# Kernel tuning notes

Hardware: AMD Instinct MI355X
Metric: run time of the kernel (lower is better)

The kernel has to match this reference:

```python
import jax, jax.numpy as jnp
import numpy as np

N_NODES = 100000
N_EDGES = 1600000
IN_DIM = 128
HID_DIM = 128
N_MASK = 5000
N_CLASSES = 4


def gcn_layer(x, src, dst, edge_weight, W, b):
    """PyG GCNConv: x' = D^{-1/2} (A + I) D^{-1/2} (x W) + b, with edge weights."""
    n = x.shape[0]
    loop = jnp.arange(n, dtype=src.dtype)
    s = jnp.concatenate([src, loop])                      # [E+N]
    d = jnp.concatenate([dst, loop])                      # [E+N]
    w = jnp.concatenate([edge_weight, jnp.ones((n,), edge_weight.dtype)])
    deg = jax.ops.segment_sum(w, d, num_segments=n)       # weighted in-degree incl. self-loop
    dis = jnp.where(deg > 0, jax.lax.rsqrt(deg), 0.0)     # deg^{-1/2}, inf -> 0
    norm = dis[s] * w * dis[d]                            # [E+N]
    h = x @ W                                             # [N, H] small GEMM
    msg = h[s] * norm[:, None]                            # gather + scale  [E+N, H]
    out = jax.ops.segment_sum(msg, d, num_segments=n)     # scatter-add     [N, H]
    return out + b


def setup_inputs() -> dict:
    key = jax.random.key(0)
    ks = jax.random.split(key, 8)
    x = jax.random.normal(ks[0], (N_NODES, IN_DIM), dtype=jnp.float32)
    edge_weight = jax.random.uniform(ks[1], (N_EDGES,), dtype=jnp.float32)
    W1 = jax.random.normal(ks[2], (IN_DIM, HID_DIM), dtype=jnp.float32) * (1.0 / np.sqrt(IN_DIM))
    b1 = jnp.zeros((HID_DIM,), jnp.float32)
    W2 = jax.random.normal(ks[3], (HID_DIM, HID_DIM), dtype=jnp.float32) * (1.0 / np.sqrt(HID_DIM))
    b2 = jnp.zeros((HID_DIM,), jnp.float32)
    edge_index = jax.random.randint(ks[4], (2, N_EDGES), 0, N_NODES, dtype=jnp.int32)
    mask_idx = jax.random.randint(ks[5], (N_MASK,), 0, N_NODES, dtype=jnp.int32)
    y = jax.random.randint(ks[6], (N_NODES,), 0, N_CLASSES, dtype=jnp.int32)
    return {"x": x, "edge_weight": edge_weight, "W1": W1, "b1": b1,
            "W2": W2, "b2": b2, "edge_index": edge_index,
            "mask_idx": mask_idx, "y": y}


def reference(x, edge_weight, W1, b1, W2, b2, edge_index, mask_idx, y):
    src, dst = edge_index[0], edge_index[1]
    h = gcn_layer(x, src, dst, edge_weight, W1, b1)
    h = jax.nn.relu(h)
    # F.dropout(training=False) in eval mode is identity
    h = gcn_layer(h, src, dst, edge_weight, W2, b2)
    return h[mask_idx], y[mask_idx]
```

## Files before the change

### kernel.cpp

```cpp
#include <hip/hip_runtime.h>

constexpr int N = 100000;
constexpr int E = 1600000;
constexpr int D = 128;
constexpr int M = 5000;

constexpr int MF_BLKS = (N + 255) / 256;

constexpr int NB  = 196;
constexpr int EB  = 2048;
constexpr int NPB = (E + EB - 1) / EB;
constexpr int HL  = NB * NPB;
constexpr int SC_BLKS = (HL + 1023) / 1024;
constexpr int PREP_BLKS = 64;
constexpr int MB_BLKS = (M + 255) / 256;

typedef __attribute__((ext_vector_type(8))) short bf16x8;
typedef __attribute__((ext_vector_type(4))) float f32x4;


__device__ __forceinline__ unsigned int pack_bf16x2(float a, float b) {
    unsigned int ua = __float_as_uint(a);
    unsigned int ub = __float_as_uint(b);
    ua = (ua + 0x7FFFu + ((ua >> 16) & 1u)) >> 16;
    ub = (ub + 0x7FFFu + ((ub >> 16) & 1u)) & 0xFFFF0000u;
    return ua | ub;
}
__device__ __forceinline__ unsigned short bf16_rne(float a) {
    unsigned int ua = __float_as_uint(a);
    return (unsigned short)((ua + 0x7FFFu + ((ua >> 16) & 1u)) >> 16);
}
__device__ __forceinline__ float bf16_lo(unsigned int u) { return __uint_as_float(u << 16); }
__device__ __forceinline__ float bf16_hi(unsigned int u) { return __uint_as_float(u & 0xFFFF0000u); }


__global__ __launch_bounds__(256) void k_misc1(const int* __restrict__ dst,
                                               int* __restrict__ hist,
                                               const float* __restrict__ W1,
                                               unsigned int* __restrict__ Wt1,
                                               const float* __restrict__ W2,
                                               unsigned int* __restrict__ Wt2,
                                               const int* __restrict__ mask,
                                               unsigned int* __restrict__ maskbit,
                                               unsigned int* __restrict__ needed) {
    __shared__ int h[NB];
    const int t = threadIdx.x;
    if (blockIdx.x < NPB) {
        if (t < NB) h[t] = 0;
        __syncthreads();
        const int base = blockIdx.x * EB;
#pragma unroll
        for (int i = 0; i < 8; ++i) {
            int e = base + t + i * 256;
            if (e < E) {
                int b = __builtin_nontemporal_load(dst + e) >> 9;
                atomicAdd(&h[b], 1);
            }
        }
        __syncthreads();
        if (t < NB) hist[t * NPB + blockIdx.x] = h[t];
    } else if (blockIdx.x < NPB + PREP_BLKS) {
        int gi = (blockIdx.x - NPB) * 256 + t;
        const float* W = (gi < 8192) ? W1 : W2;
        unsigned int* Wt = (gi < 8192) ? Wt1 : Wt2;
        int idx = gi & 8191;
        int n = idx >> 6, kk = idx & 63;
        float a = W[(2 * kk) * D + n];
        float b = W[(2 * kk + 1) * D + n];
        Wt[idx] = pack_bf16x2(a, b);
    } else {
        int i = (blockIdx.x - NPB - PREP_BLKS) * 256 + t;
        if (i < M) {
            int n = mask[i];
            atomicOr(&maskbit[n >> 5], 1u << (n & 31));
            atomicOr(&needed[n >> 5], 1u << (n & 31));
        }
    }
}


__global__ __launch_bounds__(256) void k_misc2(const int* __restrict__ hist,
                                               int* __restrict__ bs,
                                               const unsigned int* __restrict__ maskbit,
                                               const int* __restrict__ src,
                                               const int* __restrict__ dst,
                                               unsigned int* __restrict__ needed) {
    __shared__ int ws_[4];
    const int t = threadIdx.x;
    if (blockIdx.x < SC_BLKS) {
        const int idx = blockIdx.x * 1024 + t * 4;
        int s = 0;
        if (idx + 3 < HL) {
            int4 c = *(const int4*)(hist + idx);
            s = c.x + c.y + c.z + c.w;
        } else {
            for (int i = 0; i < 4; ++i) if (idx + i < HL) s += hist[idx + i];
        }
        for (int off = 32; off > 0; off >>= 1) s += __shfl_down(s, off);
        if ((t & 63) == 0) ws_[t >> 6] = s;
        __syncthreads();
        if (t == 0) bs[blockIdx.x] = ws_[0] + ws_[1] + ws_[2] + ws_[3];
    } else {
        const int base = (blockIdx.x - SC_BLKS) * EB;
#pragma unroll
        for (int i = 0; i < 8; ++i) {
            int e = base + t + i * 256;
            if (e < E) {
                int d = __builtin_nontemporal_load(dst + e);
                if ((maskbit[d >> 5] >> (d & 31)) & 1u) {
                    int s = src[e];
                    atomicOr(&needed[s >> 5], 1u << (s & 31));
                }
            }
        }
    }
}


__global__ __launch_bounds__(256) void k_scanf(const int* __restrict__ hist,
                                               const int* __restrict__ bs,
                                               int* __restrict__ histS) {
    __shared__ int sh[256];
    __shared__ int waveS[4];
    const int t = threadIdx.x;
    const int lane = t & 63;
    const int wave = t >> 6;

    sh[t] = (t < SC_BLKS) ? bs[t] : 0;
    __syncthreads();
    for (int off = 1; off < 256; off <<= 1) {
        int u = (t >= off) ? sh[t - off] : 0;
        __syncthreads();
        sh[t] += u;
        __syncthreads();
    }
    const int bOff = sh[blockIdx.x] - bs[blockIdx.x];

    const int idx = blockIdx.x * 1024 + t * 4;
    int4 c = make_int4(0, 0, 0, 0);
    if (idx + 3 < HL) c = *(const int4*)(hist + idx);
    else {
        if (idx + 0 < HL) c.x = hist[idx + 0];
        if (idx + 1 < HL) c.y = hist[idx + 1];
        if (idx + 2 < HL) c.z = hist[idx + 2];
        if (idx + 3 < HL) c.w = hist[idx + 3];
    }
    int s = c.x + c.y + c.z + c.w;

    int v = s;
    for (int off = 1; off < 64; off <<= 1) {
        int u = __shfl_up(v, off);
        if (lane >= off) v += u;
    }
    if (lane == 63) waveS[wave] = v;
    __syncthreads();
    int waveBase = 0;
    for (int w = 0; w < 4; ++w) if (w < wave) waveBase += waveS[w];
    int excl = bOff + waveBase + (v - s);

    int4 rs;
    rs.x = excl;
    rs.y = excl + c.x;
    rs.z = excl + c.x + c.y;
    rs.w = excl + c.x + c.y + c.z;
    if (idx + 3 < HL) {
        *(int4*)(histS + idx) = rs;
    } else {
        if (idx + 0 < HL) histS[idx + 0] = rs.x;
        if (idx + 1 < HL) histS[idx + 1] = rs.y;
        if (idx + 2 < HL) histS[idx + 2] = rs.z;
        if (idx + 3 < HL) histS[idx + 3] = rs.w;
    }
}


union SMem {
    unsigned int Ws[128 * 68];
    struct { int cnt[512]; float wsum[512]; int off[512]; int waveS[4]; } l;
};


template <bool BF16IN>
__device__ __forceinline__ void gemm_mfma_body(unsigned int* __restrict__ Ws,
                                               const void* __restrict__ Xin,
                                               const unsigned int* __restrict__ Wt,
                                               unsigned short* __restrict__ out, int blk) {
    const int t = threadIdx.x;
#pragma unroll
    for (int i = 0; i < 8; ++i) {
        int f4 = t + i * 256;
        int n = f4 >> 4;
        int k4 = f4 & 15;
        uint4 w = ((const uint4*)Wt)[f4];
        *(uint4*)(&Ws[n * 68 + k4 * 4]) = w;
    }
    __syncthreads();

    const int wv = t >> 6, lane = t & 63;
    const int q = lane >> 4, l15 = lane & 15;
    const int rowBase = blk * 256 + wv * 64;

    f32x4 acc[4][8] = {};
#pragma unroll
    for (int kc = 0; kc < 4; ++kc) {
        bf16x8 af[4];
#pragma unroll
        for (int rt = 0; rt < 4; ++rt) {
            int row = rowBase + rt * 16 + l15;
            if (row > N - 1) row = N - 1;
            union { uint4 u; bf16x8 v; } cv;
            if (BF16IN) {
                cv.u = *(const uint4*)((const unsigned int*)Xin + (size_t)row * 64 + kc * 16 + q * 4);
            } else {
                const float* xr = (const float*)Xin + (size_t)row * D + kc * 32 + q * 8;
                float4 x0 = *(const float4*)xr;
                float4 x1 = *(const float4*)(xr + 4);
                cv.u.x = pack_bf16x2(x0.x, x0.y);
                cv.u.y = pack_bf16x2(x0.z, x0.w);
                cv.u.z = pack_bf16x2(x1.x, x1.y);
                cv.u.w = pack_bf16x2(x1.z, x1.w);
            }
            af[rt] = cv.v;
        }
#pragma unroll
        for (int ct = 0; ct < 8; ++ct) {
            union { uint4 u; bf16x8 v; } bv;
            bv.u = *(const uint4*)(&Ws[(ct * 16 + l15) * 68 + kc * 16 + q * 4]);
#pragma unroll
            for (int rt = 0; rt < 4; ++rt)
                acc[rt][ct] = __builtin_amdgcn_mfma_f32_16x16x32_bf16(af[rt], bv.v, acc[rt][ct], 0, 0, 0);
        }
    }

#pragma unroll
    for (int rt = 0; rt < 4; ++rt) {
#pragma unroll
        for (int ct = 0; ct < 8; ++ct) {
            int col = ct * 16 + l15;
#pragma unroll
            for (int r = 0; r < 4; ++r) {
                int row = rowBase + rt * 16 + q * 4 + r;
                if (row < N) out[(size_t)row * D + col] = bf16_rne(acc[rt][ct][r]);
            }
        }
    }
}


__global__ __launch_bounds__(256) void k_part(const int* __restrict__ src,
                                              const int* __restrict__ dst,
                                              const float* __restrict__ ew,
                                              const int* __restrict__ histS,
                                              unsigned long long* __restrict__ tmp) {
    __shared__ int base_[NB];
    const int t = threadIdx.x;
    if (t < NB) base_[t] = histS[t * NPB + blockIdx.x];
    __syncthreads();
    const int eb = blockIdx.x * EB;
#pragma unroll
    for (int i = 0; i < 8; ++i) {
        int e = eb + t + i * 256;
        if (e < E) {
            int d = __builtin_nontemporal_load(dst + e);
            int s = __builtin_nontemporal_load(src + e);
            float w = __builtin_nontemporal_load(ew + e);
            int b = d >> 9;
            int pos = atomicAdd(&base_[b], 1);
            unsigned long long rec =
                ((unsigned long long)(unsigned int)__float_as_int(w) << 32) |
                ((unsigned int)s << 9) | (unsigned int)(d & 511);
            __builtin_nontemporal_store(rec, tmp + pos);
        }
    }
}


__device__ __forceinline__ void local_body(SMem& sm,
                                           const unsigned long long* __restrict__ tmp,
                                           const int* __restrict__ histS,
                                           float* __restrict__ dis,
                                           int* __restrict__ rowStart,
                                           int2* __restrict__ pairs) {
    const int b = blockIdx.x;
    const int t = threadIdx.x;
    const int segBeg = histS[b * NPB];
    const int segEnd = (b + 1 < NB) ? histS[(b + 1) * NPB] : E;

    int*   cnt   = sm.l.cnt;
    float* wsum  = sm.l.wsum;
    int*   off   = sm.l.off;
    int*   waveS = sm.l.waveS;
    cnt[t] = 0; cnt[t + 256] = 0;
    wsum[t] = 0.f; wsum[t + 256] = 0.f;
    __syncthreads();

    for (int e = segBeg + t; e < segEnd; e += 256) {
        unsigned long long rec = tmp[e];
        int dl = (int)(rec & 511);
        float w = __uint_as_float((unsigned int)(rec >> 32));
        atomicAdd(&cnt[dl], 1);
        atomicAdd(&wsum[dl], w);
    }
    __syncthreads();

    const int i0 = t * 2, i1 = t * 2 + 1;
    const int c0 = cnt[i0], c1 = cnt[i1];
    const int pv = c0 + c1;
    const int lane = t & 63, wv = t >> 6;
    int v = pv;
    for (int o = 1; o < 64; o <<= 1) {
        int u = __shfl_up(v, o);
        if (lane >= o) v += u;
    }
    if (lane == 63) waveS[wv] = v;
    __syncthreads();
    int wb = 0;
    for (int w = 0; w < 4; ++w) if (w < wv) wb += waveS[w];
    const int ex = wb + v - pv;
    off[i0] = ex;
    off[i1] = ex + c0;
    const int node0 = b * 512 + i0, node1 = b * 512 + i1;
    if (node0 < N) { rowStart[node0] = segBeg + ex;      dis[node0] = rsqrtf(1.0f + wsum[i0]); }
    if (node1 < N) { rowStart[node1] = segBeg + ex + c0; dis[node1] = rsqrtf(1.0f + wsum[i1]); }
    cnt[i0] = 0; cnt[i1] = 0;
    if (b == NB - 1 && t == 0) rowStart[N] = E;
    __syncthreads();

    for (int e = segBeg + t; e < segEnd; e += 256) {
        unsigned long long rec = tmp[e];
        int dl = (int)(rec & 511);
        int s  = (int)((rec >> 9) & 0xFFFFF);
        unsigned int wbits = (unsigned int)(rec >> 32);
        int r = atomicAdd(&cnt[dl], 1);
        pairs[segBeg + off[dl] + r] = make_int2(s, (int)wbits);
    }
}


__global__ __launch_bounds__(256) void k_local_g1(const unsigned long long* __restrict__ tmp,
                                                  const int* __restrict__ histS,
                                                  float* __restrict__ dis,
                                                  int* __restrict__ rowStart,
                                                  int2* __restrict__ pairs,
                                                  const float* __restrict__ x,
                                                  const unsigned int* __restrict__ Wt1,
                                                  unsigned short* __restrict__ A) {
    __shared__ SMem sm;
    if (blockIdx.x < NB) {
        local_body(sm, tmp, histS, dis, rowStart, pairs);
    } else {
        gemm_mfma_body<false>(sm.Ws, x, Wt1, A, blockIdx.x - NB);
    }
}

__global__ __launch_bounds__(256) void k_gemm2(const unsigned short* __restrict__ B,
                                               const unsigned int* __restrict__ Wt2,
                                               unsigned short* __restrict__ A2) {
    __shared__ SMem sm;
    gemm_mfma_body<true>(sm.Ws, B, Wt2, A2, blockIdx.x);
}


__global__ __launch_bounds__(256) void k_aggregate(const unsigned int* __restrict__ Hb,
                                                   const int2* __restrict__ pairs,
                                                   const int* __restrict__ rowStart,
                                                   const float* __restrict__ dis,
                                                   const unsigned int* __restrict__ needed,
                                                   const float* __restrict__ b,
                                                   unsigned int* __restrict__ outB) {
    int node = blockIdx.x * 4 + (threadIdx.x >> 6);
    if (node >= N) return;
    if (!((needed[node >> 5] >> (node & 31)) & 1u)) return;
    int lane = threadIdx.x & 63;
    int beg = rowStart[node], end = rowStart[node + 1];

    float ax = 0.f, ay = 0.f;
    int j = beg;
    for (; j + 7 < end; j += 8) {
        int2 p[8];
        float vv[8];
        unsigned int h[8];
#pragma unroll
        for (int i = 0; i < 8; ++i) p[i] = pairs[j + i];
#pragma unroll
        for (int i = 0; i < 8; ++i) { h[i] = Hb[(size_t)p[i].x * 64 + lane]; vv[i] = dis[p[i].x]; }
#pragma unroll
        for (int i = 0; i < 8; ++i) {
            float v = __int_as_float(p[i].y) * vv[i];
            ax += bf16_lo(h[i]) * v;
            ay += bf16_hi(h[i]) * v;
        }
    }
    for (; j + 3 < end; j += 4) {
        int2 p[4];
        float vv[4];
        unsigned int h[4];
#pragma unroll
        for (int i = 0; i < 4; ++i) p[i] = pairs[j + i];
#pragma unroll
        for (int i = 0; i < 4; ++i) { h[i] = Hb[(size_t)p[i].x * 64 + lane]; vv[i] = dis[p[i].x]; }
#pragma unroll
        for (int i = 0; i < 4; ++i) {
            float v = __int_as_float(p[i].y) * vv[i];
            ax += bf16_lo(h[i]) * v;
            ay += bf16_hi(h[i]) * v;
        }
    }
    for (; j < end; ++j) {
        int2 p0 = pairs[j];
        unsigned int h0 = Hb[(size_t)p0.x * 64 + lane];
        float v0 = __int_as_float(p0.y) * dis[p0.x];
        ax += bf16_lo(h0) * v0;
        ay += bf16_hi(h0) * v0;
    }

    float dd = dis[node];
    float sn = dd * dd;
    unsigned int hs = Hb[(size_t)node * 64 + lane];
    float2 bb = ((const float2*)b)[lane];
    float ox = fmaxf(ax * dd + bf16_lo(hs) * sn + bb.x, 0.f);
    float oy = fmaxf(ay * dd + bf16_hi(hs) * sn + bb.y, 0.f);
    __builtin_nontemporal_store(pack_bf16x2(ox, oy), outB + (size_t)node * 64 + lane);
}


__global__ __launch_bounds__(256) void k_aggregate_mask(const unsigned int* __restrict__ Hb,
                                                        const int2* __restrict__ pairs,
                                                        const int* __restrict__ rowStart,
                                                        const float* __restrict__ dis,
                                                        const float* __restrict__ b,
                                                        const int* __restrict__ mask,
                                                        const int* __restrict__ y,
                                                        float* __restrict__ out) {
    int i = blockIdx.x * 4 + (threadIdx.x >> 6);
    if (i >= M) return;
    int lane = threadIdx.x & 63;
    int node = mask[i];
    int beg = rowStart[node], end = rowStart[node + 1];

    float ax = 0.f, ay = 0.f;
    int j = beg;
    for (; j + 7 < end; j += 8) {
        int2 p[8];
        float vv[8];
        unsigned int h[8];
#pragma unroll
        for (int ii = 0; ii < 8; ++ii) p[ii] = pairs[j + ii];
#pragma unroll
        for (int ii = 0; ii < 8; ++ii) { h[ii] = Hb[(size_t)p[ii].x * 64 + lane]; vv[ii] = dis[p[ii].x]; }
#pragma unroll
        for (int ii = 0; ii < 8; ++ii) {
            float v = __int_as_float(p[ii].y) * vv[ii];
            ax += bf16_lo(h[ii]) * v;
            ay += bf16_hi(h[ii]) * v;
        }
    }
    for (; j < end; ++j) {
        int2 p0 = pairs[j];
        unsigned int h0 = Hb[(size_t)p0.x * 64 + lane];
        float v0 = __int_as_float(p0.y) * dis[p0.x];
        ax += bf16_lo(h0) * v0;
        ay += bf16_hi(h0) * v0;
    }

    float dd = dis[node];
    float sn = dd * dd;
    unsigned int hs = Hb[(size_t)node * 64 + lane];
    float2 bb = ((const float2*)b)[lane];
    float ox = ax * dd + bf16_lo(hs) * sn + bb.x;
    float oy = ay * dd + bf16_hi(hs) * sn + bb.y;
    ((float2*)(out + (size_t)i * D))[lane] = make_float2(ox, oy);
    if (lane == 0) out[(size_t)M * D + i] = (float)y[node];
}

extern "C" void kernel_launch(void* const* d_in, const int* in_sizes, int n_in,
                              void* d_out, int out_size, void* d_ws, size_t ws_size,
                              hipStream_t stream) {
    const float* x  = (const float*)d_in[0];
    const float* ew = (const float*)d_in[1];
    const float* W1 = (const float*)d_in[2];
    const float* b1 = (const float*)d_in[3];
    const float* W2 = (const float*)d_in[4];
    const float* b2 = (const float*)d_in[5];
    const int* eidx = (const int*)d_in[6];
    const int* mask = (const int*)d_in[7];
    const int* y    = (const int*)d_in[8];
    const int* src = eidx;
    const int* dst = eidx + E;

    char* ws = (char*)d_ws;
    float* dis      = (float*)(ws);
    int*   rowStart = (int*)(ws + (size_t)512 * 1024);
    int*   scanBS   = (int*)(ws + (size_t)1024 * 1024);
    unsigned int* maskbit = (unsigned int*)(ws + (size_t)1056 * 1024);
    unsigned int* needed  = (unsigned int*)(ws + (size_t)1072 * 1024);
    unsigned int* Wt1 = (unsigned int*)(ws + (size_t)1088 * 1024);
    unsigned int* Wt2 = (unsigned int*)(ws + (size_t)1120 * 1024);
    int*   hist     = (int*)(ws + (size_t)1280 * 1024);
    int*   histS    = (int*)(ws + (size_t)1920 * 1024);
    int2*  pairs    = (int2*)(ws + (size_t)3 * 1024 * 1024);
    unsigned long long* tmp = (unsigned long long*)(ws + (size_t)16 * 1024 * 1024);
    unsigned short* A  = (unsigned short*)(ws + (size_t)29 * 1024 * 1024);
    unsigned short* B  = (unsigned short*)(ws + (size_t)55 * 1024 * 1024);
    unsigned short* A2 = (unsigned short*)(ws + (size_t)81 * 1024 * 1024);

    (void)hipMemsetAsync(maskbit, 0, (size_t)32 * 1024, stream);
    hipLaunchKernelGGL(k_misc1, dim3(NPB + PREP_BLKS + MB_BLKS), dim3(256), 0, stream,
                       dst, hist, W1, Wt1, W2, Wt2, mask, maskbit, needed);

    hipLaunchKernelGGL(k_misc2, dim3(SC_BLKS + NPB), dim3(256), 0, stream,
                       hist, scanBS, maskbit, src, dst, needed);
    hipLaunchKernelGGL(k_scanf, dim3(SC_BLKS), dim3(256), 0, stream, hist, scanBS, histS);

    hipLaunchKernelGGL(k_part, dim3(NPB), dim3(256), 0, stream,
                       src, dst, ew, histS, tmp);
    hipLaunchKernelGGL(k_local_g1, dim3(NB + MF_BLKS), dim3(256), 0, stream,
                       tmp, histS, dis, rowStart, pairs, x, Wt1, A);

    hipLaunchKernelGGL(k_aggregate, dim3((N + 3) / 4), dim3(256), 0, stream,
                       (const unsigned int*)A, pairs, rowStart, dis, needed, b1,
                       (unsigned int*)B);

    hipLaunchKernelGGL(k_gemm2, dim3(MF_BLKS), dim3(256), 0, stream, B, Wt2, A2);
    hipLaunchKernelGGL(k_aggregate_mask, dim3((M + 3) / 4), dim3(256), 0, stream,
                       (const unsigned int*)A2, pairs, rowStart, dis, b2, mask, y, (float*)d_out);
}
```

Before: 288.4 us.

## Shrink destination buckets to 128 nodes for finer-grained local sort

Reduces the destination bucket size from 512 to 128 nodes, so there are about 782 buckets instead of 196. That gives more blocks in the local CSR-build phase and less per-block shared-memory atomic work. The histogram becomes four times larger, so the scan kernels now process 16 entries per thread and the workspace offsets are shifted, with A2 aliased onto A. The costs are more histogram traffic and scattered partition writes across more buckets, and the A2 aliasing relies on A being dead by the time A2 is written.

```diff
diff --git a/kernel.cpp b/kernel.cpp
--- a/kernel.cpp
+++ b/kernel.cpp
@@ -7,11 +7,14 @@
 
 constexpr int MF_BLKS = (N + 255) / 256;
 
-constexpr int NB  = 196;
+constexpr int NBITS = 7;
+constexpr int BUCKET = 1 << NBITS;
+constexpr int NB  = (N + BUCKET - 1) / BUCKET;
 constexpr int EB  = 2048;
 constexpr int NPB = (E + EB - 1) / EB;
 constexpr int HL  = NB * NPB;
-constexpr int SC_BLKS = (HL + 1023) / 1024;
+constexpr int SCCH = 4096;
+constexpr int SC_BLKS = (HL + SCCH - 1) / SCCH;
 constexpr int PREP_BLKS = 64;
 constexpr int MB_BLKS = (M + 255) / 256;
 
@@ -46,19 +49,19 @@
     __shared__ int h[NB];
     const int t = threadIdx.x;
     if (blockIdx.x < NPB) {
-        if (t < NB) h[t] = 0;
+        for (int i = t; i < NB; i += 256) h[i] = 0;
         __syncthreads();
         const int base = blockIdx.x * EB;
 #pragma unroll
         for (int i = 0; i < 8; ++i) {
             int e = base + t + i * 256;
             if (e < E) {
-                int b = __builtin_nontemporal_load(dst + e) >> 9;
+                int b = __builtin_nontemporal_load(dst + e) >> NBITS;
                 atomicAdd(&h[b], 1);
             }
         }
         __syncthreads();
-        if (t < NB) hist[t * NPB + blockIdx.x] = h[t];
+        for (int i = t; i < NB; i += 256) hist[i * NPB + blockIdx.x] = h[i];
     } else if (blockIdx.x < NPB + PREP_BLKS) {
         int gi = (blockIdx.x - NPB) * 256 + t;
         const float* W = (gi < 8192) ? W1 : W2;
@@ -88,13 +91,16 @@
     __shared__ int ws_[4];
     const int t = threadIdx.x;
     if (blockIdx.x < SC_BLKS) {
-        const int idx = blockIdx.x * 1024 + t * 4;
+        const int idx = blockIdx.x * SCCH + t * 16;
         int s = 0;
-        if (idx + 3 < HL) {
-            int4 c = *(const int4*)(hist + idx);
-            s = c.x + c.y + c.z + c.w;
+        if (idx + 15 < HL) {
+#pragma unroll
+            for (int g = 0; g < 4; ++g) {
+                int4 c = *(const int4*)(hist + idx + g * 4);
+                s += c.x + c.y + c.z + c.w;
+            }
         } else {
-            for (int i = 0; i < 4; ++i) if (idx + i < HL) s += hist[idx + i];
+            for (int g = 0; g < 16; ++g) if (idx + g < HL) s += hist[idx + g];
         }
         for (int off = 32; off > 0; off >>= 1) s += __shfl_down(s, off);
         if ((t & 63) == 0) ws_[t >> 6] = s;
@@ -136,16 +142,21 @@
     }
     const int bOff = sh[blockIdx.x] - bs[blockIdx.x];
 
-    const int idx = blockIdx.x * 1024 + t * 4;
-    int4 c = make_int4(0, 0, 0, 0);
-    if (idx + 3 < HL) c = *(const int4*)(hist + idx);
-    else {
-        if (idx + 0 < HL) c.x = hist[idx + 0];
-        if (idx + 1 < HL) c.y = hist[idx + 1];
-        if (idx + 2 < HL) c.z = hist[idx + 2];
-        if (idx + 3 < HL) c.w = hist[idx + 3];
-    }
-    int s = c.x + c.y + c.z + c.w;
+    const int idx = blockIdx.x * SCCH + t * 16;
+    int c[16];
+    if (idx + 15 < HL) {
+#pragma unroll
+        for (int g = 0; g < 4; ++g) {
+            int4 q = *(const int4*)(hist + idx + g * 4);
+            c[g * 4 + 0] = q.x; c[g * 4 + 1] = q.y; c[g * 4 + 2] = q.z; c[g * 4 + 3] = q.w;
+        }
+    } else {
+#pragma unroll
+        for (int g = 0; g < 16; ++g) c[g] = (idx + g < HL) ? hist[idx + g] : 0;
+    }
+    int s = 0;
+#pragma unroll
+    for (int g = 0; g < 16; ++g) s += c[g];
 
     int v = s;
     for (int off = 1; off < 64; off <<= 1) {
@@ -158,25 +169,24 @@
     for (int w = 0; w < 4; ++w) if (w < wave) waveBase += waveS[w];
     int excl = bOff + waveBase + (v - s);
 
-    int4 rs;
-    rs.x = excl;
-    rs.y = excl + c.x;
-    rs.z = excl + c.x + c.y;
-    rs.w = excl + c.x + c.y + c.z;
-    if (idx + 3 < HL) {
-        *(int4*)(histS + idx) = rs;
+    int rs[16];
+    int run = excl;
+#pragma unroll
+    for (int g = 0; g < 16; ++g) { rs[g] = run; run += c[g]; }
+    if (idx + 15 < HL) {
+#pragma unroll
+        for (int g = 0; g < 4; ++g)
+            *(int4*)(histS + idx + g * 4) = make_int4(rs[g * 4], rs[g * 4 + 1], rs[g * 4 + 2], rs[g * 4 + 3]);
     } else {
-        if (idx + 0 < HL) histS[idx + 0] = rs.x;
-        if (idx + 1 < HL) histS[idx + 1] = rs.y;
-        if (idx + 2 < HL) histS[idx + 2] = rs.z;
-        if (idx + 3 < HL) histS[idx + 3] = rs.w;
+#pragma unroll
+        for (int g = 0; g < 16; ++g) if (idx + g < HL) histS[idx + g] = rs[g];
     }
 }
 
 
 union SMem {
     unsigned int Ws[128 * 68];
-    struct { int cnt[512]; float wsum[512]; int off[512]; int waveS[4]; } l;
+    struct { int cnt[BUCKET]; float wsum[BUCKET]; int off[BUCKET]; int waveS[2]; } l;
 };
 
 
@@ -254,7 +264,7 @@
                                               unsigned long long* __restrict__ tmp) {
     __shared__ int base_[NB];
     const int t = threadIdx.x;
-    if (t < NB) base_[t] = histS[t * NPB + blockIdx.x];
+    for (int i = t; i < NB; i += 256) base_[i] = histS[i * NPB + blockIdx.x];
     __syncthreads();
     const int eb = blockIdx.x * EB;
 #pragma unroll
@@ -264,11 +274,11 @@
             int d = __builtin_nontemporal_load(dst + e);
             int s = __builtin_nontemporal_load(src + e);
             float w = __builtin_nontemporal_load(ew + e);
-            int b = d >> 9;
+            int b = d >> NBITS;
             int pos = atomicAdd(&base_[b], 1);
             unsigned long long rec =
                 ((unsigned long long)(unsigned int)__float_as_int(w) << 32) |
-                ((unsigned int)s << 9) | (unsigned int)(d & 511);
+                ((unsigned int)s << NBITS) | (unsigned int)(d & (BUCKET - 1));
             __builtin_nontemporal_store(rec, tmp + pos);
         }
     }
@@ -290,46 +300,42 @@
     float* wsum  = sm.l.wsum;
     int*   off   = sm.l.off;
     int*   waveS = sm.l.waveS;
-    cnt[t] = 0; cnt[t + 256] = 0;
-    wsum[t] = 0.f; wsum[t + 256] = 0.f;
+    if (t < BUCKET) { cnt[t] = 0; wsum[t] = 0.f; }
     __syncthreads();
 
     for (int e = segBeg + t; e < segEnd; e += 256) {
         unsigned long long rec = tmp[e];
-        int dl = (int)(rec & 511);
+        int dl = (int)(rec & (BUCKET - 1));
         float w = __uint_as_float((unsigned int)(rec >> 32));
         atomicAdd(&cnt[dl], 1);
         atomicAdd(&wsum[dl], w);
     }
     __syncthreads();
 
-    const int i0 = t * 2, i1 = t * 2 + 1;
-    const int c0 = cnt[i0], c1 = cnt[i1];
-    const int pv = c0 + c1;
     const int lane = t & 63, wv = t >> 6;
+    const int pv = (t < BUCKET) ? cnt[t] : 0;
     int v = pv;
     for (int o = 1; o < 64; o <<= 1) {
         int u = __shfl_up(v, o);
         if (lane >= o) v += u;
     }
-    if (lane == 63) waveS[wv] = v;
-    __syncthreads();
-    int wb = 0;
-    for (int w = 0; w < 4; ++w) if (w < wv) wb += waveS[w];
-    const int ex = wb + v - pv;
-    off[i0] = ex;
-    off[i1] = ex + c0;
-    const int node0 = b * 512 + i0, node1 = b * 512 + i1;
-    if (node0 < N) { rowStart[node0] = segBeg + ex;      dis[node0] = rsqrtf(1.0f + wsum[i0]); }
-    if (node1 < N) { rowStart[node1] = segBeg + ex + c0; dis[node1] = rsqrtf(1.0f + wsum[i1]); }
-    cnt[i0] = 0; cnt[i1] = 0;
+    if (lane == 63 && wv < 2) waveS[wv] = v;
+    __syncthreads();
+    if (t < BUCKET) {
+        const int wb = (wv == 1) ? waveS[0] : 0;
+        const int ex = wb + v - pv;
+        off[t] = ex;
+        const int node = b * BUCKET + t;
+        if (node < N) { rowStart[node] = segBeg + ex; dis[node] = rsqrtf(1.0f + wsum[t]); }
+        cnt[t] = 0;
+    }
     if (b == NB - 1 && t == 0) rowStart[N] = E;
     __syncthreads();
 
     for (int e = segBeg + t; e < segEnd; e += 256) {
         unsigned long long rec = tmp[e];
-        int dl = (int)(rec & 511);
-        int s  = (int)((rec >> 9) & 0xFFFFF);
+        int dl = (int)(rec & (BUCKET - 1));
+        int s  = (int)((rec >> NBITS) & 0xFFFFF);
         unsigned int wbits = (unsigned int)(rec >> 32);
         int r = atomicAdd(&cnt[dl], 1);
         pairs[segBeg + off[dl] + r] = make_int2(s, (int)wbits);
@@ -497,12 +503,12 @@
     unsigned int* Wt1 = (unsigned int*)(ws + (size_t)1088 * 1024);
     unsigned int* Wt2 = (unsigned int*)(ws + (size_t)1120 * 1024);
     int*   hist     = (int*)(ws + (size_t)1280 * 1024);
-    int*   histS    = (int*)(ws + (size_t)1920 * 1024);
-    int2*  pairs    = (int2*)(ws + (size_t)3 * 1024 * 1024);
-    unsigned long long* tmp = (unsigned long long*)(ws + (size_t)16 * 1024 * 1024);
-    unsigned short* A  = (unsigned short*)(ws + (size_t)29 * 1024 * 1024);
-    unsigned short* B  = (unsigned short*)(ws + (size_t)55 * 1024 * 1024);
-    unsigned short* A2 = (unsigned short*)(ws + (size_t)81 * 1024 * 1024);
+    int*   histS    = (int*)(ws + (size_t)3968 * 1024);
+    int2*  pairs    = (int2*)(ws + (size_t)6656 * 1024);
+    unsigned long long* tmp = (unsigned long long*)(ws + (size_t)19968 * 1024);
+    unsigned short* A  = (unsigned short*)(ws + (size_t)33 * 1024 * 1024);
+    unsigned short* B  = (unsigned short*)(ws + (size_t)59 * 1024 * 1024);
+    unsigned short* A2 = A;
 
     (void)hipMemsetAsync(maskbit, 0, (size_t)32 * 1024, stream);
     hipLaunchKernelGGL(k_misc1, dim3(NPB + PREP_BLKS + MB_BLKS), dim3(256), 0, stream,
```

Result: slower. 301.4 us (+4.5%).
